# Kernel optimization log

Measured on AMD Instinct MI355X. Metric: run time of the kernel, lower is better.

Reference implementation:

```python
import jax, jax.numpy as jnp
import numpy as np

N, E, H, F = 100000, 1000000, 4, 64
D_IN = 64


def _gat_conv(x, src, dst, W, al, ar, b, act):
    # x: [N, D_in], W: [D_in, H*F], al/ar: [H, F], b: [H, F]
    z = (x @ W).reshape(N, H, F)
    el = jnp.sum(z * al, axis=-1)              # [N, H]
    er = jnp.sum(z * ar, axis=-1)              # [N, H]
    e = jax.nn.leaky_relu(el[src] + er[dst], 0.2)   # [E, H]
    # edge softmax over incoming edges of each dst node
    m = jax.ops.segment_max(e, dst, num_segments=N)  # [N, H]
    ex = jnp.exp(e - m[dst])                         # [E, H]
    s = jax.ops.segment_sum(ex, dst, num_segments=N)  # [N, H]
    alpha = ex / s[dst]                              # [E, H]
    msg = z[src] * alpha[..., None]                  # [E, H, F] (largest intermediate)
    out = jax.ops.segment_sum(msg, dst, num_segments=N) + b  # [N, H, F]
    return act(out)


def setup_inputs() -> dict:
    key = jax.random.key(0)
    ks = jax.random.split(key, 12)
    sc_in = 1.0 / np.sqrt(D_IN)
    sc_f = 1.0 / np.sqrt(F)
    return {
        "x": jax.random.normal(ks[0], (N, D_IN), jnp.float32),
        "src": jax.random.randint(ks[1], (E,), 0, N, jnp.int32),
        "dst": jax.random.randint(ks[2], (E,), 0, N, jnp.int32),
        "W1": jax.random.normal(ks[3], (D_IN, H * F), jnp.float32) * sc_in,
        "al1": jax.random.normal(ks[4], (H, F), jnp.float32) * sc_f,
        "ar1": jax.random.normal(ks[5], (H, F), jnp.float32) * sc_f,
        "b1": jnp.zeros((H, F), jnp.float32),
        "W2": jax.random.normal(ks[6], (F, H * F), jnp.float32) * sc_f,
        "al2": jax.random.normal(ks[7], (H, F), jnp.float32) * sc_f,
        "ar2": jax.random.normal(ks[8], (H, F), jnp.float32) * sc_f,
        "b2": jnp.zeros((H, F), jnp.float32),
    }


def reference(x, src, dst, W1, al1, ar1, b1, W2, al2, ar2, b2):
    # layer 1: GATConv with tanh activation, then mean over heads
    h = _gat_conv(x, src, dst, W1, al1, ar1, b1, jnp.tanh)   # [N, H, F]
    h = h.mean(axis=-2)                                      # [N, F]
    # layer 2: GATConv (no activation), then mean over heads
    h = _gat_conv(h, src, dst, W2, al2, ar2, b2, lambda v: v)
    return h.mean(axis=-2)                                   # [N, F]
```

## Files before the change

kernel.cpp:

```cpp
#include <hip/hip_runtime.h>

typedef _Float16 f16x8 __attribute__((ext_vector_type(8)));
typedef _Float16 f16x4 __attribute__((ext_vector_type(4)));
typedef float f32x4 __attribute__((ext_vector_type(4)));

#define PADB 16
#define MAXNB 512
#define TILE_A 4096

__device__ __forceinline__ float lrelu(float v) { return v >= 0.f ? v : 0.2f * v; }
__device__ __forceinline__ float cexp(float v) { return expf(fminf(v, 60.f)); }
__device__ __forceinline__ float ftanh(float x) {
    float e = __expf(fminf(2.f * x, 30.f));
    return (e - 1.f) / (e + 1.f);
}

__global__ __launch_bounds__(256) void k_wprep(
    const float* __restrict__ W1, const float* __restrict__ al1, const float* __restrict__ ar1,
    const float* __restrict__ W2, const float* __restrict__ al2, const float* __restrict__ ar2,
    float* __restrict__ A1l, float* __restrict__ A1r,
    float* __restrict__ A2l, float* __restrict__ A2r,
    _Float16* __restrict__ Wt1, _Float16* __restrict__ Wt2,
    int* __restrict__ bktc, int nb)
{
    int b = blockIdx.x, t = threadIdx.x;
    if (b < 2) {
        const float* W  = b ? W2 : W1;
        const float* al = b ? al2 : al1;
        const float* ar = b ? ar2 : ar1;
        float* Al = b ? A2l : A1l;
        float* Ar = b ? A2r : A1r;
        _Float16* Wt = b ? Wt2 : Wt1;
        int k = t >> 2, h = t & 3;
        float sl = 0.f, sr = 0.f;
#pragma unroll 8
        for (int f = 0; f < 64; ++f) {
            float wv = W[k * 256 + h * 64 + f];
            sl = fmaf(wv, al[h * 64 + f], sl);
            sr = fmaf(wv, ar[h * 64 + f], sr);
        }
        Al[k * 4 + h] = sl;
        Ar[k * 4 + h] = sr;
        int col = t;
#pragma unroll 8
        for (int kk = 0; kk < 64; ++kk)
            Wt[col * 64 + kk] = (_Float16)W[kk * 256 + col];
    } else {
        for (int i = t; i < nb; i += 256) bktc[(size_t)i * PADB] = 0;
    }
}

__global__ __launch_bounds__(256) void k_elr_hist(
    const float* __restrict__ Xf, _Float16* __restrict__ XhOut,
    const float* __restrict__ Al, const float* __restrict__ Ar,
    float* __restrict__ el, float* __restrict__ er, int nNodes,
    const int* __restrict__ dst, int* __restrict__ bktc, int E_, int ebBlocks,
    int nb)
{
    int b = blockIdx.x;
    if (b < ebBlocks) {
        __shared__ int lb[MAXNB];
        int t = threadIdx.x;
        for (int i = t; i < nb; i += 256) lb[i] = 0;
        __syncthreads();
        int base = b * TILE_A;
        int end = base + TILE_A; if (end > E_) end = E_;
        for (int j = base + t; j < end; j += 256)
            atomicAdd(&lb[((unsigned)dst[j]) >> 8], 1);
        __syncthreads();
        for (int i = t; i < nb; i += 256) {
            int c = lb[i];
            if (c) atomicAdd(&bktc[(size_t)i * PADB], c);
        }
        return;
    }
    int lane = threadIdx.x & 63, wid = threadIdx.x >> 6;
    int q = lane >> 4, c = lane & 15;
    int n = (b - ebBlocks) * 16 + wid * 4 + q;
    if (n >= nNodes) return;
    float4 xv = *reinterpret_cast<const float4*>(Xf + (size_t)n * 64 + c * 4);
    f16x4 xh4 = {(_Float16)xv.x, (_Float16)xv.y, (_Float16)xv.z, (_Float16)xv.w};
    *reinterpret_cast<f16x4*>(XhOut + (size_t)n * 64 + c * 4) = xh4;
    float p0 = 0.f, p1 = 0.f, p2 = 0.f, p3 = 0.f;
    float q0 = 0.f, q1 = 0.f, q2 = 0.f, q3 = 0.f;
    float xs[4] = {xv.x, xv.y, xv.z, xv.w};
#pragma unroll
    for (int i = 0; i < 4; ++i) {
        float4 av = *reinterpret_cast<const float4*>(Al + (c * 4 + i) * 4);
        float4 rv = *reinterpret_cast<const float4*>(Ar + (c * 4 + i) * 4);
        p0 = fmaf(xs[i], av.x, p0); p1 = fmaf(xs[i], av.y, p1);
        p2 = fmaf(xs[i], av.z, p2); p3 = fmaf(xs[i], av.w, p3);
        q0 = fmaf(xs[i], rv.x, q0); q1 = fmaf(xs[i], rv.y, q1);
        q2 = fmaf(xs[i], rv.z, q2); q3 = fmaf(xs[i], rv.w, q3);
    }
#pragma unroll
    for (int m = 1; m <= 8; m <<= 1) {
        p0 += __shfl_xor(p0, m, 64); p1 += __shfl_xor(p1, m, 64);
        p2 += __shfl_xor(p2, m, 64); p3 += __shfl_xor(p3, m, 64);
        q0 += __shfl_xor(q0, m, 64); q1 += __shfl_xor(q1, m, 64);
        q2 += __shfl_xor(q2, m, 64); q3 += __shfl_xor(q3, m, 64);
    }
    if (c == 0) {
        *reinterpret_cast<float4*>(el + (size_t)n * 4) = make_float4(p0, p1, p2, p3);
        *reinterpret_cast<float4*>(er + (size_t)n * 4) = make_float4(q0, q1, q2, q3);
    }
}

__global__ __launch_bounds__(256) void k_elr2(
    const _Float16* __restrict__ Xh,
    const float* __restrict__ Al, const float* __restrict__ Ar,
    float* __restrict__ el, float* __restrict__ er, int nNodes)
{
    int lane = threadIdx.x & 63, wid = threadIdx.x >> 6;
    int q = lane >> 4, c = lane & 15;
    int n = blockIdx.x * 16 + wid * 4 + q;
    if (n >= nNodes) return;
    f16x4 xh4 = *reinterpret_cast<const f16x4*>(Xh + (size_t)n * 64 + c * 4);
    float p0 = 0.f, p1 = 0.f, p2 = 0.f, p3 = 0.f;
    float q0 = 0.f, q1 = 0.f, q2 = 0.f, q3 = 0.f;
#pragma unroll
    for (int i = 0; i < 4; ++i) {
        float xs = (float)xh4[i];
        float4 av = *reinterpret_cast<const float4*>(Al + (c * 4 + i) * 4);
        float4 rv = *reinterpret_cast<const float4*>(Ar + (c * 4 + i) * 4);
        p0 = fmaf(xs, av.x, p0); p1 = fmaf(xs, av.y, p1);
        p2 = fmaf(xs, av.z, p2); p3 = fmaf(xs, av.w, p3);
        q0 = fmaf(xs, rv.x, q0); q1 = fmaf(xs, rv.y, q1);
        q2 = fmaf(xs, rv.z, q2); q3 = fmaf(xs, rv.w, q3);
    }
#pragma unroll
    for (int m = 1; m <= 8; m <<= 1) {
        p0 += __shfl_xor(p0, m, 64); p1 += __shfl_xor(p1, m, 64);
        p2 += __shfl_xor(p2, m, 64); p3 += __shfl_xor(p3, m, 64);
        q0 += __shfl_xor(q0, m, 64); q1 += __shfl_xor(q1, m, 64);
        q2 += __shfl_xor(q2, m, 64); q3 += __shfl_xor(q3, m, 64);
    }
    if (c == 0) {
        *reinterpret_cast<float4*>(el + (size_t)n * 4) = make_float4(p0, p1, p2, p3);
        *reinterpret_cast<float4*>(er + (size_t)n * 4) = make_float4(q0, q1, q2, q3);
    }
}

__global__ void k_bscan(const int* __restrict__ bktc, int* __restrict__ bbase,
                        int* __restrict__ bcur, int nb) {
    int lane = threadIdx.x;
    int carry = 0;
    for (int base = 0; base < nb; base += 64) {
        int i = base + lane;
        int v = (i < nb) ? bktc[(size_t)i * PADB] : 0;
        int sc = v;
#pragma unroll
        for (int d = 1; d < 64; d <<= 1) {
            int u = __shfl_up(sc, d, 64);
            if (lane >= d) sc += u;
        }
        if (i < nb) {
            int ex = carry + sc - v;
            bbase[i] = ex;
            bcur[(size_t)i * PADB] = ex;
        }
        carry += __shfl(sc, 63, 64);
    }
    if (lane == 0) bbase[nb] = carry;
}

__global__ __launch_bounds__(256) void k_binA(
    const int* __restrict__ src, const int* __restrict__ dst,
    int* __restrict__ bcur, unsigned* __restrict__ ebkt, int E_, int nb)
{
    __shared__ int lcnt[MAXNB];
    __shared__ int lcur[MAXNB];
    __shared__ int lofs[MAXNB];
    __shared__ int gbase[MAXNB];
    __shared__ unsigned spack[TILE_A];
    __shared__ int gposs[TILE_A];
    int t = threadIdx.x;
    int tile0 = blockIdx.x * TILE_A;
    int cntT = E_ - tile0; if (cntT > TILE_A) cntT = TILE_A;

    for (int i = t; i < nb; i += 256) { lcnt[i] = 0; lcur[i] = 0; }
    __syncthreads();

    int myS[16], myD[16];
#pragma unroll
    for (int k = 0; k < 16; ++k) {
        int idx = k * 256 + t;
        if (idx < cntT) {
            myS[k] = src[tile0 + idx];
            myD[k] = dst[tile0 + idx];
            atomicAdd(&lcnt[((unsigned)myD[k]) >> 8], 1);
        }
    }
    __syncthreads();

    for (int i = t; i < nb; i += 256) {
        int c = lcnt[i];
        gbase[i] = c ? atomicAdd(&bcur[(size_t)i * PADB], c) : 0;
    }
    if (t < 64) {
        int carry = 0;
        for (int base = 0; base < nb; base += 64) {
            int i = base + t;
            int v = (i < nb) ? lcnt[i] : 0;
            int sc = v;
#pragma unroll
            for (int d = 1; d < 64; d <<= 1) {
                int u = __shfl_up(sc, d, 64);
                if (t >= d) sc += u;
            }
            if (i < nb) lofs[i] = carry + sc - v;
            carry += __shfl(sc, 63, 64);
        }
    }
    __syncthreads();

#pragma unroll
    for (int k = 0; k < 16; ++k) {
        int idx = k * 256 + t;
        if (idx < cntT) {
            int b = ((unsigned)myD[k]) >> 8;
            int slot = atomicAdd(&lcur[b], 1);
            int lidx = lofs[b] + slot;
            spack[lidx] = (unsigned)myS[k] | (((unsigned)myD[k] & 255u) << 17);
            gposs[lidx] = gbase[b] + slot;
        }
    }
    __syncthreads();

    for (int j = t; j < cntT; j += 256)
        ebkt[gposs[j]] = spack[j];
}

__global__ __launch_bounds__(256) void k_binC(
    const unsigned* __restrict__ ebkt, const int* __restrict__ bbase,
    int* __restrict__ cnt, int nNodes)
{
    __shared__ int lc[256];
    int b = blockIdx.x, t = threadIdx.x;
    lc[t] = 0;
    __syncthreads();
    int s0 = bbase[b], s1 = bbase[b + 1];
    for (int j = s0 + t; j < s1; j += 256)
        atomicAdd(&lc[ebkt[j] >> 17], 1);
    __syncthreads();
    int node = (b << 8) + t;
    if (node < nNodes) cnt[node] = lc[t];
}

__global__ __launch_bounds__(256) void k_binB(
    const unsigned* __restrict__ ebkt, const int* __restrict__ bbase,
    const int* __restrict__ offs, int* __restrict__ esrc, int nNodes)
{
    __shared__ int lcur[256];
    __shared__ int lofs[256];
    int b = blockIdx.x, t = threadIdx.x;
    lcur[t] = 0;
    int node = (b << 8) + t;
    lofs[t] = (node < nNodes) ? offs[node] : 0;
    __syncthreads();
    int s0 = bbase[b], s1 = bbase[b + 1];
    for (int j = s0 + t; j < s1; j += 256) {
        unsigned v = ebkt[j];
        int dl = v >> 17;
        int p = lofs[dl] + atomicAdd(&lcur[dl], 1);
        esrc[p] = (int)(v & 0x1FFFFu);
    }
}

#define SC_VPT 8
#define SC_CHUNK 2048

__global__ __launch_bounds__(256) void k_chunk_sums(const int* __restrict__ cnt,
                                                    int* __restrict__ bsums, int n) {
    int tid = threadIdx.x;
    int base = blockIdx.x * SC_CHUNK + tid * SC_VPT;
    int s = 0;
#pragma unroll
    for (int i = 0; i < SC_VPT; ++i) { int idx = base + i; if (idx < n) s += cnt[idx]; }
#pragma unroll
    for (int m = 1; m < 64; m <<= 1) s += __shfl_xor(s, m, 64);
    int lane = tid & 63, wid = tid >> 6;
    __shared__ int sh[4];
    if (lane == 0) sh[wid] = s;
    __syncthreads();
    if (tid == 0) bsums[blockIdx.x] = sh[0] + sh[1] + sh[2] + sh[3];
}

__global__ void k_scan_mid(int* bsums, int nb) {
    int lane = threadIdx.x & 63;
    int carry = 0;
    for (int base = 0; base < nb; base += 64) {
        int i = base + lane;
        int v = (i < nb) ? bsums[i] : 0;
        int sc = v;
#pragma unroll
        for (int d = 1; d < 64; d <<= 1) {
            int t = __shfl_up(sc, d, 64);
            if (lane >= d) sc += t;
        }
        if (i < nb) bsums[i] = carry + sc - v;
        carry += __shfl(sc, 63, 64);
    }
}

__global__ __launch_bounds__(256) void k_scan_write(const int* __restrict__ cnt,
                                                    const int* __restrict__ bsums,
                                                    int* __restrict__ offs, int n) {
    int tid = threadIdx.x;
    int base = blockIdx.x * SC_CHUNK + tid * SC_VPT;
    int v[SC_VPT]; int s = 0;
#pragma unroll
    for (int i = 0; i < SC_VPT; ++i) { int idx = base + i; v[i] = (idx < n) ? cnt[idx] : 0; s += v[i]; }
    int lane = tid & 63, wid = tid >> 6;
    int sc = s;
#pragma unroll
    for (int d = 1; d < 64; d <<= 1) { int t = __shfl_up(sc, d, 64); if (lane >= d) sc += t; }
    __shared__ int wsum[4];
    if (lane == 63) wsum[wid] = sc;
    __syncthreads();
    int wbase = 0;
    for (int i = 0; i < wid; ++i) wbase += wsum[i];
    int p = bsums[blockIdx.x] + wbase + (sc - s);
#pragma unroll
    for (int i = 0; i < SC_VPT; ++i) {
        int idx = base + i;
        if (idx < n) {
            offs[idx] = p; p += v[i];
            if (idx == n - 1) offs[n] = p;
        }
    }
}

template <typename OutT>
__global__ __launch_bounds__(256) void k_sgp(
    const int* __restrict__ esrc, const int* __restrict__ offs,
    const float* __restrict__ el, const float* __restrict__ er,
    const _Float16* __restrict__ Xh,
    const _Float16* __restrict__ Wt, const float* __restrict__ B,
    OutT* __restrict__ out, int nNodes, int do_tanh)
{
    __shared__ _Float16 sagg[16 * 264];
    int tid = threadIdx.x;
    int lane = tid & 63, wid = tid >> 6;
    int q = lane >> 4, c = lane & 15, c4 = c * 4;
    int n = blockIdx.x * 16 + wid * 4 + q;
    int nl = wid * 4 + q;
    bool valid = n < nNodes;

    float A0[4] = {}, A1[4] = {}, A2[4] = {}, A3[4] = {};
    if (valid) {
        int s0 = offs[n], s1 = offs[n + 1];
        int d = s1 - s0;
        float4 erv = *reinterpret_cast<const float4*>(er + (size_t)n * 4);

        int sreg = 0;
        float x0 = 0.f, x1 = 0.f, x2 = 0.f, x3 = 0.f;
        if (c < d) {
            sreg = esrc[s0 + c];
            float4 v = *reinterpret_cast<const float4*>(el + (size_t)sreg * 4);
            x0 = cexp(lrelu(v.x + erv.x)); x1 = cexp(lrelu(v.y + erv.y));
            x2 = cexp(lrelu(v.z + erv.z)); x3 = cexp(lrelu(v.w + erv.w));
        }
        float t0 = x0, t1 = x1, t2 = x2, t3 = x3;
        for (int j = s0 + c + 16; j < s1; j += 16) {
            int s = esrc[j];
            float4 v = *reinterpret_cast<const float4*>(el + (size_t)s * 4);
            t0 += cexp(lrelu(v.x + erv.x)); t1 += cexp(lrelu(v.y + erv.y));
            t2 += cexp(lrelu(v.z + erv.z)); t3 += cexp(lrelu(v.w + erv.w));
        }
#pragma unroll
        for (int m = 1; m <= 8; m <<= 1) {
            t0 += __shfl_xor(t0, m, 64); t1 += __shfl_xor(t1, m, 64);
            t2 += __shfl_xor(t2, m, 64); t3 += __shfl_xor(t3, m, 64);
        }
        float i0 = 1.f / t0, i1 = 1.f / t1, i2 = 1.f / t2, i3 = 1.f / t3;
        float a0 = x0 * i0, a1 = x1 * i1, a2 = x2 * i2, a3 = x3 * i3;

        int base = s0;
        bool first = true;
        while (base < s1) {
            int cnt_ = s1 - base; if (cnt_ > 16) cnt_ = 16;
            int sj; float w0, w1, w2, w3;
            if (first) { sj = sreg; w0 = a0; w1 = a1; w2 = a2; w3 = a3; }
            else {
                sj = 0; w0 = w1 = w2 = w3 = 0.f;
                if (c < cnt_) {
                    sj = esrc[base + c];
                    float4 v = *reinterpret_cast<const float4*>(el + (size_t)sj * 4);
                    w0 = cexp(lrelu(v.x + erv.x)) * i0;
                    w1 = cexp(lrelu(v.y + erv.y)) * i1;
                    w2 = cexp(lrelu(v.z + erv.z)) * i2;
                    w3 = cexp(lrelu(v.w + erv.w)) * i3;
                }
            }
            int rnd = (cnt_ + 3) & ~3;
            for (int b = 0; b < rnd; b += 4) {
                int ss[4];
                float q0[4], q1[4], q2[4], q3[4];
                f16x4 xv[4];
#pragma unroll
                for (int u = 0; u < 4; ++u) {
                    int jj = q * 16 + b + u;
                    ss[u] = __shfl(sj, jj, 64);
                    q0[u] = __shfl(w0, jj, 64); q1[u] = __shfl(w1, jj, 64);
                    q2[u] = __shfl(w2, jj, 64); q3[u] = __shfl(w3, jj, 64);
                }
#pragma unroll
                for (int u = 0; u < 4; ++u)
                    xv[u] = *reinterpret_cast<const f16x4*>(Xh + (size_t)ss[u] * 64 + c4);
#pragma unroll
                for (int u = 0; u < 4; ++u) {
#pragma unroll
                    for (int i = 0; i < 4; ++i) {
                        float xf = (float)xv[u][i];
                        A0[i] = fmaf(q0[u], xf, A0[i]);
                        A1[i] = fmaf(q1[u], xf, A1[i]);
                        A2[i] = fmaf(q2[u], xf, A2[i]);
                        A3[i] = fmaf(q3[u], xf, A3[i]);
                    }
                }
            }
            base += 16; first = false;
        }
    }
    {
        _Float16* aggr = sagg + nl * 264;
        f16x4 h0, h1v, h2, h3;
#pragma unroll
        for (int i = 0; i < 4; ++i) {
            h0[i] = (_Float16)A0[i]; h1v[i] = (_Float16)A1[i];
            h2[i] = (_Float16)A2[i]; h3[i] = (_Float16)A3[i];
        }
        *reinterpret_cast<f16x4*>(aggr + c4)       = h0;
        *reinterpret_cast<f16x4*>(aggr + 64 + c4)  = h1v;
        *reinterpret_cast<f16x4*>(aggr + 128 + c4) = h2;
        *reinterpret_cast<f16x4*>(aggr + 192 + c4) = h3;
    }

    int col = c, quad = q, f0 = wid * 16;
    f16x8 bfrag[4][2];
    float bias[4];
#pragma unroll
    for (int h = 0; h < 4; ++h) {
#pragma unroll
        for (int ks = 0; ks < 2; ++ks)
            bfrag[h][ks] = *reinterpret_cast<const f16x8*>(
                Wt + (h * 64 + f0 + col) * 64 + ks * 32 + quad * 8);
        bias[h] = B[h * 64 + f0 + col];
    }
    __syncthreads();

    const _Float16* ap = sagg + col * 264 + quad * 8;
    f32x4 acc = {0.f, 0.f, 0.f, 0.f};
#pragma unroll
    for (int h = 0; h < 4; ++h) {
        f16x8 a0 = *reinterpret_cast<const f16x8*>(ap + h * 64);
        f16x8 a1 = *reinterpret_cast<const f16x8*>(ap + h * 64 + 32);
        f32x4 dd = {0.f, 0.f, 0.f, 0.f};
        dd = __builtin_amdgcn_mfma_f32_16x16x32_f16(a0, bfrag[h][0], dd, 0, 0, 0);
        dd = __builtin_amdgcn_mfma_f32_16x16x32_f16(a1, bfrag[h][1], dd, 0, 0, 0);
        if (do_tanh) {
#pragma unroll
            for (int r = 0; r < 4; ++r) acc[r] += ftanh(dd[r] + bias[h]);
        } else {
#pragma unroll
            for (int r = 0; r < 4; ++r) acc[r] += dd[r] + bias[h];
        }
    }
    int n0 = blockIdx.x * 16;
#pragma unroll
    for (int r = 0; r < 4; ++r) {
        int row = n0 + quad * 4 + r;
        if (row < nNodes)
            out[(size_t)row * 64 + f0 + col] = (OutT)(0.25f * acc[r]);
    }
}

extern "C" void kernel_launch(void* const* d_in, const int* in_sizes, int n_in,
                              void* d_out, int out_size, void* d_ws, size_t ws_size,
                              hipStream_t stream) {
    const float* x   = (const float*)d_in[0];
    const int*   src = (const int*)d_in[1];
    const int*   dst = (const int*)d_in[2];
    const float* W1  = (const float*)d_in[3];
    const float* al1 = (const float*)d_in[4];
    const float* ar1 = (const float*)d_in[5];
    const float* b1  = (const float*)d_in[6];
    const float* W2  = (const float*)d_in[7];
    const float* al2 = (const float*)d_in[8];
    const float* ar2 = (const float*)d_in[9];
    const float* b2  = (const float*)d_in[10];
    float* out = (float*)d_out;

    int N_ = in_sizes[0] / 64;
    int E_ = in_sizes[1];
    int NB_ = (N_ + 255) >> 8;

    char* ws = (char*)d_ws;
    size_t off = 0;
    auto alloc = [&](size_t bytes) -> void* {
        void* p = ws + off;
        off = (off + bytes + 255) & ~(size_t)255;
        return p;
    };
    _Float16* xh  = (_Float16*)alloc(((size_t)N_ + 16) * 64 * 2);
    _Float16* h1h = (_Float16*)alloc(((size_t)N_ + 16) * 64 * 2);
    float* el   = (float*)alloc(((size_t)N_ + 16) * 4 * 4);
    float* er   = (float*)alloc(((size_t)N_ + 16) * 4 * 4);
    int*   cnt  = (int*)alloc((size_t)(N_ + 16) * 4);
    int*   offs = (int*)alloc((size_t)(N_ + 1) * 4);
    int*   esrc = (int*)alloc((size_t)E_ * 4);
    unsigned* ebkt = (unsigned*)alloc((size_t)E_ * 4);
    int*   bktc = (int*)alloc((size_t)MAXNB * PADB * 4);
    int*   bcur = (int*)alloc((size_t)MAXNB * PADB * 4);
    int*   bbase= (int*)alloc((size_t)(MAXNB + 1) * 4);
    int*   bsums= (int*)alloc(4096);
    float* A1l  = (float*)alloc(64 * 4 * 4);
    float* A1r  = (float*)alloc(64 * 4 * 4);
    float* A2l  = (float*)alloc(64 * 4 * 4);
    float* A2r  = (float*)alloc(64 * 4 * 4);
    _Float16* Wt1 = (_Float16*)alloc(256 * 64 * 2);
    _Float16* Wt2 = (_Float16*)alloc(256 * 64 * 2);

    k_wprep<<<3, 256, 0, stream>>>(W1, al1, ar1, W2, al2, ar2,
                                   A1l, A1r, A2l, A2r, Wt1, Wt2, bktc, NB_);

    int hb = (E_ + TILE_A - 1) / TILE_A;
    int nb16 = (N_ + 15) / 16;
    k_elr_hist<<<hb + nb16, 256, 0, stream>>>(x, xh, A1l, A1r, el, er, N_,
                                              dst, bktc, E_, hb, NB_);
    k_bscan<<<1, 64, 0, stream>>>(bktc, bbase, bcur, NB_);
    k_binA<<<hb, 256, 0, stream>>>(src, dst, bcur, ebkt, E_, NB_);
    k_binC<<<NB_, 256, 0, stream>>>(ebkt, bbase, cnt, N_);
    int nchunks = (N_ + SC_CHUNK - 1) / SC_CHUNK;
    k_chunk_sums<<<nchunks, 256, 0, stream>>>(cnt, bsums, N_);
    k_scan_mid<<<1, 64, 0, stream>>>(bsums, nchunks);
    k_scan_write<<<nchunks, 256, 0, stream>>>(cnt, bsums, offs, N_);
    k_binB<<<NB_, 256, 0, stream>>>(ebkt, bbase, offs, esrc, N_);

    k_sgp<_Float16><<<nb16, 256, 0, stream>>>(esrc, offs, el, er, xh,
                                              Wt1, b1, h1h, N_, 1);
    k_elr2<<<nb16, 256, 0, stream>>>(h1h, A2l, A2r, el, er, N_);
    k_sgp<float><<<nb16, 256, 0, stream>>>(esrc, offs, el, er, h1h,
                                           Wt2, b2, out, N_, 0);
}
```

Baseline: 276.6 us.

## Fully unroll first 16-edge chunk with packed fp16 weights and fast exp

The first 16 incoming edges of each node are now processed in one fully unrolled block that issues all 16 row gathers at once, which raises memory-level parallelism for the typical low-degree node. Attention weights are packed into fp16 pairs to halve the shuffle count, and cexp switches to the fast __expf intrinsic. Launch bounds now request 4 blocks per SM to limit register growth. Risks are register pressure or spills from the 16-entry arrays, and reduced precision in the fp16 alpha weights and the fast exp.

After: 277.3 us. Within noise of the previous version (+0.2%).

```diff
diff --git a/kernel.cpp b/kernel.cpp
--- a/kernel.cpp
+++ b/kernel.cpp
@@ -2,6 +2,7 @@
 
 typedef _Float16 f16x8 __attribute__((ext_vector_type(8)));
 typedef _Float16 f16x4 __attribute__((ext_vector_type(4)));
+typedef _Float16 f16x2 __attribute__((ext_vector_type(2)));
 typedef float f32x4 __attribute__((ext_vector_type(4)));
 
 #define PADB 16
@@ -9,7 +10,7 @@
 #define TILE_A 4096
 
 __device__ __forceinline__ float lrelu(float v) { return v >= 0.f ? v : 0.2f * v; }
-__device__ __forceinline__ float cexp(float v) { return expf(fminf(v, 60.f)); }
+__device__ __forceinline__ float cexp(float v) { return __expf(fminf(v, 60.f)); }
 __device__ __forceinline__ float ftanh(float x) {
     float e = __expf(fminf(2.f * x, 30.f));
     return (e - 1.f) / (e + 1.f);
@@ -332,7 +333,7 @@
 }
 
 template <typename OutT>
-__global__ __launch_bounds__(256) void k_sgp(
+__global__ __launch_bounds__(256, 4) void k_sgp(
     const int* __restrict__ esrc, const int* __restrict__ offs,
     const float* __restrict__ el, const float* __restrict__ er,
     const _Float16* __restrict__ Xh,
@@ -374,45 +375,72 @@
             t2 += __shfl_xor(t2, m, 64); t3 += __shfl_xor(t3, m, 64);
         }
         float i0 = 1.f / t0, i1 = 1.f / t1, i2 = 1.f / t2, i3 = 1.f / t3;
-        float a0 = x0 * i0, a1 = x1 * i1, a2 = x2 * i2, a3 = x3 * i3;
-
-        int base = s0;
-        bool first = true;
-        while (base < s1) {
+
+        int pk01 = 0, pk23 = 0;
+        if (c < d) {
+            f16x2 pa = {(_Float16)(x0 * i0), (_Float16)(x1 * i1)};
+            f16x2 pb = {(_Float16)(x2 * i2), (_Float16)(x3 * i3)};
+            pk01 = __builtin_bit_cast(int, pa);
+            pk23 = __builtin_bit_cast(int, pb);
+        }
+
+        int ss[16], wpa[16], wpb[16];
+#pragma unroll
+        for (int e = 0; e < 16; ++e) {
+            int jj = q * 16 + e;
+            ss[e]  = __shfl(sreg, jj, 64);
+            wpa[e] = __shfl(pk01, jj, 64);
+            wpb[e] = __shfl(pk23, jj, 64);
+        }
+        f16x4 xv[16];
+#pragma unroll
+        for (int e = 0; e < 16; ++e)
+            xv[e] = *reinterpret_cast<const f16x4*>(Xh + (size_t)ss[e] * 64 + c4);
+#pragma unroll
+        for (int e = 0; e < 16; ++e) {
+            f16x2 wa = __builtin_bit_cast(f16x2, wpa[e]);
+            f16x2 wb = __builtin_bit_cast(f16x2, wpb[e]);
+#pragma unroll
+            for (int i = 0; i < 4; ++i) {
+                float xf = (float)xv[e][i];
+                A0[i] = fmaf((float)wa[0], xf, A0[i]);
+                A1[i] = fmaf((float)wa[1], xf, A1[i]);
+                A2[i] = fmaf((float)wb[0], xf, A2[i]);
+                A3[i] = fmaf((float)wb[1], xf, A3[i]);
+            }
+        }
+
+        for (int base = s0 + 16; base < s1; base += 16) {
             int cnt_ = s1 - base; if (cnt_ > 16) cnt_ = 16;
-            int sj; float w0, w1, w2, w3;
-            if (first) { sj = sreg; w0 = a0; w1 = a1; w2 = a2; w3 = a3; }
-            else {
-                sj = 0; w0 = w1 = w2 = w3 = 0.f;
-                if (c < cnt_) {
-                    sj = esrc[base + c];
-                    float4 v = *reinterpret_cast<const float4*>(el + (size_t)sj * 4);
-                    w0 = cexp(lrelu(v.x + erv.x)) * i0;
-                    w1 = cexp(lrelu(v.y + erv.y)) * i1;
-                    w2 = cexp(lrelu(v.z + erv.z)) * i2;
-                    w3 = cexp(lrelu(v.w + erv.w)) * i3;
-                }
+            int sj = 0; float w0 = 0.f, w1 = 0.f, w2 = 0.f, w3 = 0.f;
+            if (c < cnt_) {
+                sj = esrc[base + c];
+                float4 v = *reinterpret_cast<const float4*>(el + (size_t)sj * 4);
+                w0 = cexp(lrelu(v.x + erv.x)) * i0;
+                w1 = cexp(lrelu(v.y + erv.y)) * i1;
+                w2 = cexp(lrelu(v.z + erv.z)) * i2;
+                w3 = cexp(lrelu(v.w + erv.w)) * i3;
             }
             int rnd = (cnt_ + 3) & ~3;
             for (int b = 0; b < rnd; b += 4) {
-                int ss[4];
+                int ssr[4];
                 float q0[4], q1[4], q2[4], q3[4];
-                f16x4 xv[4];
+                f16x4 xr[4];
 #pragma unroll
                 for (int u = 0; u < 4; ++u) {
                     int jj = q * 16 + b + u;
-                    ss[u] = __shfl(sj, jj, 64);
+                    ssr[u] = __shfl(sj, jj, 64);
                     q0[u] = __shfl(w0, jj, 64); q1[u] = __shfl(w1, jj, 64);
                     q2[u] = __shfl(w2, jj, 64); q3[u] = __shfl(w3, jj, 64);
                 }
 #pragma unroll
                 for (int u = 0; u < 4; ++u)
-                    xv[u] = *reinterpret_cast<const f16x4*>(Xh + (size_t)ss[u] * 64 + c4);
+                    xr[u] = *reinterpret_cast<const f16x4*>(Xh + (size_t)ssr[u] * 64 + c4);
 #pragma unroll
                 for (int u = 0; u < 4; ++u) {
 #pragma unroll
                     for (int i = 0; i < 4; ++i) {
-                        float xf = (float)xv[u][i];
+                        float xf = (float)xr[u][i];
                         A0[i] = fmaf(q0[u], xf, A0[i]);
                         A1[i] = fmaf(q1[u], xf, A1[i]);
                         A2[i] = fmaf(q2[u], xf, A2[i]);
@@ -420,7 +448,6 @@
                     }
                 }
             }
-            base += 16; first = false;
         }
     }
     {
```

## Broadcast per-edge source and fp16 weights via LDS instead of shuffles

Applied to the files above, without the earlier changes.

Replaces the 20 cross-lane shuffles per 4-edge group with each lane writing its edge's source index and fp16-packed attention weights into a shared int4 slot, then reading four slots back as broadcasts. The goal is to cut shuffle/permute cost in the gather-aggregate loop. It also switches expf to the fast __expf and adds a min-blocks launch bound of 4 to raise occupancy. Packing the weights to fp16 costs precision. There is no explicit barrier between the LDS write and read; lanes of the same wavefront share the slots, so this relies on wavefront-level execution order.

New measurement: 275.7 us. No clear change (-0.3%).

```diff
diff --git a/kernel.cpp b/kernel.cpp
--- a/kernel.cpp
+++ b/kernel.cpp
@@ -2,6 +2,7 @@
 
 typedef _Float16 f16x8 __attribute__((ext_vector_type(8)));
 typedef _Float16 f16x4 __attribute__((ext_vector_type(4)));
+typedef _Float16 f16x2 __attribute__((ext_vector_type(2)));
 typedef float f32x4 __attribute__((ext_vector_type(4)));
 
 #define PADB 16
@@ -9,7 +10,7 @@
 #define TILE_A 4096
 
 __device__ __forceinline__ float lrelu(float v) { return v >= 0.f ? v : 0.2f * v; }
-__device__ __forceinline__ float cexp(float v) { return expf(fminf(v, 60.f)); }
+__device__ __forceinline__ float cexp(float v) { return __expf(fminf(v, 60.f)); }
 __device__ __forceinline__ float ftanh(float x) {
     float e = __expf(fminf(2.f * x, 30.f));
     return (e - 1.f) / (e + 1.f);
@@ -332,7 +333,7 @@
 }
 
 template <typename OutT>
-__global__ __launch_bounds__(256) void k_sgp(
+__global__ __launch_bounds__(256, 4) void k_sgp(
     const int* __restrict__ esrc, const int* __restrict__ offs,
     const float* __restrict__ el, const float* __restrict__ er,
     const _Float16* __restrict__ Xh,
@@ -340,6 +341,7 @@
     OutT* __restrict__ out, int nNodes, int do_tanh)
 {
     __shared__ _Float16 sagg[16 * 264];
+    __shared__ int4 sedge[16][17];
     int tid = threadIdx.x;
     int lane = tid & 63, wid = tid >> 6;
     int q = lane >> 4, c = lane & 15, c4 = c * 4;
@@ -374,53 +376,54 @@
             t2 += __shfl_xor(t2, m, 64); t3 += __shfl_xor(t3, m, 64);
         }
         float i0 = 1.f / t0, i1 = 1.f / t1, i2 = 1.f / t2, i3 = 1.f / t3;
-        float a0 = x0 * i0, a1 = x1 * i1, a2 = x2 * i2, a3 = x3 * i3;
-
-        int base = s0;
-        bool first = true;
-        while (base < s1) {
+
+        for (int base = s0; base < s1; base += 16) {
             int cnt_ = s1 - base; if (cnt_ > 16) cnt_ = 16;
-            int sj; float w0, w1, w2, w3;
-            if (first) { sj = sreg; w0 = a0; w1 = a1; w2 = a2; w3 = a3; }
-            else {
-                sj = 0; w0 = w1 = w2 = w3 = 0.f;
-                if (c < cnt_) {
-                    sj = esrc[base + c];
-                    float4 v = *reinterpret_cast<const float4*>(el + (size_t)sj * 4);
-                    w0 = cexp(lrelu(v.x + erv.x)) * i0;
-                    w1 = cexp(lrelu(v.y + erv.y)) * i1;
-                    w2 = cexp(lrelu(v.z + erv.z)) * i2;
-                    w3 = cexp(lrelu(v.w + erv.w)) * i3;
+            int sj = 0, pk01 = 0, pk23 = 0;
+            if (base == s0) {
+                if (c < d) {
+                    sj = sreg;
+                    f16x2 pa = {(_Float16)(x0 * i0), (_Float16)(x1 * i1)};
+                    f16x2 pb = {(_Float16)(x2 * i2), (_Float16)(x3 * i3)};
+                    pk01 = __builtin_bit_cast(int, pa);
+                    pk23 = __builtin_bit_cast(int, pb);
                 }
+            } else if (c < cnt_) {
+                sj = esrc[base + c];
+                float4 v = *reinterpret_cast<const float4*>(el + (size_t)sj * 4);
+                f16x2 pa = {(_Float16)(cexp(lrelu(v.x + erv.x)) * i0),
+                            (_Float16)(cexp(lrelu(v.y + erv.y)) * i1)};
+                f16x2 pb = {(_Float16)(cexp(lrelu(v.z + erv.z)) * i2),
+                            (_Float16)(cexp(lrelu(v.w + erv.w)) * i3)};
+                pk01 = __builtin_bit_cast(int, pa);
+                pk23 = __builtin_bit_cast(int, pb);
             }
+            sedge[nl][c] = make_int4(sj, pk01, pk23, 0);
             int rnd = (cnt_ + 3) & ~3;
             for (int b = 0; b < rnd; b += 4) {
-                int ss[4];
-                float q0[4], q1[4], q2[4], q3[4];
+                int4 ed[4];
                 f16x4 xv[4];
 #pragma unroll
+                for (int u = 0; u < 4; ++u)
+                    ed[u] = sedge[nl][b + u];
+#pragma unroll
+                for (int u = 0; u < 4; ++u)
+                    xv[u] = *reinterpret_cast<const f16x4*>(
+                        Xh + (size_t)(unsigned)ed[u].x * 64 + c4);
+#pragma unroll
                 for (int u = 0; u < 4; ++u) {
-                    int jj = q * 16 + b + u;
-                    ss[u] = __shfl(sj, jj, 64);
-                    q0[u] = __shfl(w0, jj, 64); q1[u] = __shfl(w1, jj, 64);
-                    q2[u] = __shfl(w2, jj, 64); q3[u] = __shfl(w3, jj, 64);
-                }
-#pragma unroll
-                for (int u = 0; u < 4; ++u)
-                    xv[u] = *reinterpret_cast<const f16x4*>(Xh + (size_t)ss[u] * 64 + c4);
-#pragma unroll
-                for (int u = 0; u < 4; ++u) {
+                    f16x2 wa = __builtin_bit_cast(f16x2, ed[u].y);
+                    f16x2 wb = __builtin_bit_cast(f16x2, ed[u].z);
 #pragma unroll
                     for (int i = 0; i < 4; ++i) {
                         float xf = (float)xv[u][i];
-                        A0[i] = fmaf(q0[u], xf, A0[i]);
-                        A1[i] = fmaf(q1[u], xf, A1[i]);
-                        A2[i] = fmaf(q2[u], xf, A2[i]);
-                        A3[i] = fmaf(q3[u], xf, A3[i]);
+                        A0[i] = fmaf((float)wa[0], xf, A0[i]);
+                        A1[i] = fmaf((float)wa[1], xf, A1[i]);
+                        A2[i] = fmaf((float)wb[0], xf, A2[i]);
+                        A3[i] = fmaf((float)wb[1], xf, A3[i]);
                     }
                 }
             }
-            base += 16; first = false;
         }
     }
     {
```
